# Performance work log

Measured on AMD Instinct MI355X. Metric: run time of the kernel, lower is better.

The kernel has to match this reference:

```python
import jax, jax.numpy as jnp
import numpy as np

N, E = 50000, 800000
IN, HID, H, OUT = 128, 32, 4, 32
NEG_SLOPE = 0.2


def _gatv2_layer(x, edge_index, Wl, bl, Wr, br, att, bias, heads, ch, concat):
    """One GATv2Conv layer (PyG semantics: add self-loops, lin_l on source,
    lin_r on target, e = att . leaky_relu(gl_src + gr_dst), segment softmax
    over incoming edges of each target, scatter-add weighted source messages)."""
    n = x.shape[0]
    loop = jnp.arange(n)
    src = jnp.concatenate([edge_index[0], loop])
    dst = jnp.concatenate([edge_index[1], loop])

    gl = (x @ Wl + bl).reshape(n, heads, ch)   # source transform [N,H,C]
    gr = (x @ Wr + br).reshape(n, heads, ch)   # target transform [N,H,C]

    m = jax.nn.leaky_relu(gl[src] + gr[dst], NEG_SLOPE)   # [E+N,H,C]
    e = jnp.einsum('ehc,hc->eh', m, att)                   # [E+N,H]

    # numerically stable segment softmax over dst
    emax = jax.lax.stop_gradient(jax.ops.segment_max(e, dst, num_segments=n))
    ex = jnp.exp(e - emax[dst])
    denom = jax.ops.segment_sum(ex, dst, num_segments=n)
    alpha = ex / denom[dst]                                # [E+N,H]

    out = jax.ops.segment_sum(alpha[:, :, None] * gl[src], dst, num_segments=n)  # [N,H,C]
    out = out.reshape(n, heads * ch) if concat else out.mean(axis=1)
    return out + bias


def setup_inputs() -> dict:
    key = jax.random.key(0)
    ks = jax.random.split(key, 16)
    s = 0.05
    return {
        'x': jax.random.normal(ks[0], (N, IN), dtype=jnp.float32),
        'edge_index': jax.random.randint(ks[1], (2, E), 0, N, dtype=jnp.int32),
        # layer 1: IN -> HID, H heads, concat
        'Wl1': jax.random.normal(ks[2], (IN, H * HID), dtype=jnp.float32) * s,
        'bl1': jnp.zeros((H * HID,), dtype=jnp.float32),
        'Wr1': jax.random.normal(ks[3], (IN, H * HID), dtype=jnp.float32) * s,
        'br1': jnp.zeros((H * HID,), dtype=jnp.float32),
        'att1': jax.random.normal(ks[4], (H, HID), dtype=jnp.float32) * s,
        'bias1': jnp.zeros((H * HID,), dtype=jnp.float32),
        # layer 2: H*HID -> OUT, 1 head, no concat
        'Wl2': jax.random.normal(ks[5], (H * HID, OUT), dtype=jnp.float32) * s,
        'bl2': jnp.zeros((OUT,), dtype=jnp.float32),
        'Wr2': jax.random.normal(ks[6], (H * HID, OUT), dtype=jnp.float32) * s,
        'br2': jnp.zeros((OUT,), dtype=jnp.float32),
        'att2': jax.random.normal(ks[7], (1, OUT), dtype=jnp.float32) * s,
        'bias2': jnp.zeros((OUT,), dtype=jnp.float32),
    }


def reference(x, edge_index, Wl1, bl1, Wr1, br1, att1, bias1,
              Wl2, bl2, Wr2, br2, att2, bias2):
    h = jax.nn.elu(_gatv2_layer(x, edge_index, Wl1, bl1, Wr1, br1, att1, bias1, H, HID, True))
    # dropout inactive in eval mode
    return _gatv2_layer(h, edge_index, Wl2, bl2, Wr2, br2, att2, bias2, 1, OUT, False)
```

## Files before the change

### kernel.cpp

```cpp
#include <hip/hip_runtime.h>

#define NNODES 50000
#define NEDGES 800000
#define ETOT   (NNODES + NEDGES)
#define NEG 0.2f
#define BKTS 196
#define P1E 4096
#define NP1 ((ETOT + P1E - 1) / P1E)

typedef unsigned short ushort_t;
typedef unsigned int uint_t;
typedef __attribute__((ext_vector_type(8))) short short8;
typedef __attribute__((ext_vector_type(4))) float f32x4;

__device__ __forceinline__ ushort_t f2bf(float f) {
  uint_t u = __float_as_uint(f);
  u += 0x7FFFu + ((u >> 16) & 1u);
  return (ushort_t)(u >> 16);
}
__device__ __forceinline__ float bf2f(ushort_t h) {
  return __uint_as_float((uint_t)h << 16);
}

__global__ __launch_bounds__(256) void coarse_hist(const int* __restrict__ ei,
                                                   int* __restrict__ pcnt) {
  __shared__ int c[BKTS];
  for (int i = threadIdx.x; i < BKTS; i += 256) c[i] = 0;
  __syncthreads();
  int e0 = blockIdx.x * P1E;
#pragma unroll
  for (int t = 0; t < P1E / 256; ++t) {
    int i = e0 + t * 256 + (int)threadIdx.x;
    if (i < ETOT) {
      int dst = (i < NEDGES) ? ei[NEDGES + i] : (i - NEDGES);
      atomicAdd(&c[dst >> 8], 1);
    }
  }
  __syncthreads();
  for (int i = threadIdx.x; i < BKTS; i += 256)
    pcnt[i * NP1 + blockIdx.x] = c[i];
}

__global__ __launch_bounds__(64) void coarse_scan(const int* __restrict__ pcnt,
                                                  int* __restrict__ goffArr,
                                                  int* __restrict__ tot) {
  int b = blockIdx.x;
  int lane = threadIdx.x;
  int carry = 0;
  for (int k0 = 0; k0 < NP1; k0 += 64) {
    int k = k0 + lane;
    int v = (k < NP1) ? pcnt[b * NP1 + k] : 0;
    int s = v;
    for (int off = 1; off < 64; off <<= 1) {
      int u = __shfl_up(s, off);
      if (lane >= off) s += u;
    }
    if (k < NP1) goffArr[b * NP1 + k] = carry + s - v;
    carry += __shfl(s, 63);
  }
  if (lane == 0) tot[b] = carry;
}

__global__ __launch_bounds__(256) void bucket_scan(const int* __restrict__ tot,
                                                   int* __restrict__ bucketStart,
                                                   int* __restrict__ rowptr) {
  if (threadIdx.x == 0) {
    int r = 0;
    for (int i = 0; i < BKTS; ++i) { bucketStart[i] = r; r += tot[i]; }
    bucketStart[BKTS] = r;
    rowptr[NNODES] = ETOT;
  }
}

__global__ __launch_bounds__(256) void bin_phase1(const int* __restrict__ ei,
                                                  const int* __restrict__ bucketStart,
                                                  const int* __restrict__ goffArr,
                                                  uint_t* __restrict__ binned) {
  __shared__ int cnt[BKTS], pref[BKTS], fillL[BKTS];
  __shared__ uint_t stage[P1E];
  int e0 = blockIdx.x * P1E;
  for (int i = threadIdx.x; i < BKTS; i += 256) { cnt[i] = 0; fillL[i] = 0; }
  __syncthreads();
  uint_t mypk[P1E / 256];
  int mybkt[P1E / 256];
#pragma unroll
  for (int t = 0; t < P1E / 256; ++t) {
    int i = e0 + t * 256 + (int)threadIdx.x;
    if (i < ETOT) {
      int dst = (i < NEDGES) ? ei[NEDGES + i] : (i - NEDGES);
      int src = (i < NEDGES) ? ei[i] : dst;
      int b = dst >> 8;
      mypk[t] = (uint_t)src | ((uint_t)(dst & 255) << 16) | ((uint_t)b << 24);
      mybkt[t] = b;
      atomicAdd(&cnt[b], 1);
    } else mybkt[t] = -1;
  }
  __syncthreads();
  if (threadIdx.x == 0) {
    int r = 0;
    for (int b = 0; b < BKTS; ++b) { pref[b] = r; r += cnt[b]; }
  }
  __syncthreads();
#pragma unroll
  for (int t = 0; t < P1E / 256; ++t) {
    if (mybkt[t] >= 0) {
      int p = pref[mybkt[t]] + atomicAdd(&fillL[mybkt[t]], 1);
      stage[p] = mypk[t];
    }
  }
  __syncthreads();
  int total = (e0 + P1E <= ETOT) ? P1E : (ETOT - e0);
  for (int j = threadIdx.x; j < total; j += 256) {
    uint_t pk = stage[j];
    int b = pk >> 24;
    binned[bucketStart[b] + goffArr[b * NP1 + blockIdx.x] + (j - pref[b])] = pk;
  }
}

__global__ __launch_bounds__(256) void bin_phase2(const uint_t* __restrict__ binned,
                                                  const int* __restrict__ bucketStart,
                                                  int* __restrict__ rowptr,
                                                  int* __restrict__ csrc) {
  __shared__ int cnt[256], pref[256], fillL[256];
  __shared__ int outS[8192];
  int b = blockIdx.x;
  int base = bucketStart[b];
  int cntAll = bucketStart[b + 1] - base;
  cnt[threadIdx.x] = 0; fillL[threadIdx.x] = 0;
  __syncthreads();
  for (int j = threadIdx.x; j < cntAll; j += 256)
    atomicAdd(&cnt[(binned[base + j] >> 16) & 255], 1);
  __syncthreads();
  if (threadIdx.x == 0) {
    int r = 0;
    for (int i = 0; i < 256; ++i) { pref[i] = r; r += cnt[i]; }
  }
  __syncthreads();
  int node = b * 256 + (int)threadIdx.x;
  if (node < NNODES) rowptr[node] = base + pref[threadIdx.x];
  for (int j = threadIdx.x; j < cntAll; j += 256) {
    uint_t pk = binned[base + j];
    int d = (pk >> 16) & 255;
    int p = pref[d] + atomicAdd(&fillL[d], 1);
    outS[p] = (int)(pk & 0xFFFF);
  }
  __syncthreads();
  for (int j = threadIdx.x; j < cntAll; j += 256)
    csrc[base + j] = outS[j];
}

__global__ __launch_bounds__(256) void prep_w(const float* __restrict__ Wl1,
                                              const float* __restrict__ Wr1,
                                              ushort_t* __restrict__ WtHi,
                                              ushort_t* __restrict__ WtLo) {
  int k = blockIdx.x;
  int n = threadIdx.x;
  float w = (n < 128) ? Wl1[k * 128 + n] : Wr1[k * 128 + (n - 128)];
  ushort_t h = f2bf(w);
  WtHi[n * 128 + k] = h;
  WtLo[n * 128 + k] = f2bf(w - bf2f(h));
}

__global__ __launch_bounds__(256) void gemm1_mfma(
    const float* __restrict__ x,
    const ushort_t* __restrict__ WtHi, const ushort_t* __restrict__ WtLo,
    const float* __restrict__ bl1, const float* __restrict__ br1,
    ushort_t* __restrict__ gl1, ushort_t* __restrict__ gr1) {
  constexpr int LDA = 132;
  __shared__ __align__(16) char smem[32 * 260 * 4];
  ushort_t (*Ahi)[LDA] = (ushort_t(*)[LDA])smem;
  ushort_t (*Alo)[LDA] = (ushort_t(*)[LDA])(smem + 32 * LDA * 2);
  float (*Cs)[260] = (float(*)[260])smem;
  int m0 = blockIdx.x * 32;
  int tid = threadIdx.x;
#pragma unroll
  for (int i = 0; i < 4; ++i) {
    int it = i * 256 + tid;
    int row = it >> 5, c4 = it & 31;
    int gm = m0 + row;
    float4 v = (gm < NNODES) ? *(const float4*)&x[(size_t)gm * 128 + 4 * c4]
                             : make_float4(0.f, 0.f, 0.f, 0.f);
    ushort_t h0 = f2bf(v.x), h1 = f2bf(v.y), h2 = f2bf(v.z), h3 = f2bf(v.w);
    ushort_t l0 = f2bf(v.x - bf2f(h0)), l1 = f2bf(v.y - bf2f(h1));
    ushort_t l2 = f2bf(v.z - bf2f(h2)), l3 = f2bf(v.w - bf2f(h3));
    uint2 ph, pl;
    ph.x = (uint_t)h0 | ((uint_t)h1 << 16); ph.y = (uint_t)h2 | ((uint_t)h3 << 16);
    pl.x = (uint_t)l0 | ((uint_t)l1 << 16); pl.y = (uint_t)l2 | ((uint_t)l3 << 16);
    *(uint2*)&Ahi[row][4 * c4] = ph;
    *(uint2*)&Alo[row][4 * c4] = pl;
  }
  __syncthreads();
  int wave = tid >> 6, lane = tid & 63;
  int quad = lane >> 4, nl = lane & 15;
  int nb = wave * 64;
  f32x4 acc[2][4];
#pragma unroll
  for (int tm = 0; tm < 2; ++tm)
#pragma unroll
    for (int tn = 0; tn < 4; ++tn) acc[tm][tn] = (f32x4){0.f, 0.f, 0.f, 0.f};

#pragma unroll
  for (int kc = 0; kc < 4; ++kc) {
    int klane = kc * 32 + quad * 8;
    short8 ah[2], al[2], bh[4], bl[4];
#pragma unroll
    for (int tm = 0; tm < 2; ++tm) {
      ah[tm] = *(const short8*)&Ahi[16 * tm + nl][klane];
      al[tm] = *(const short8*)&Alo[16 * tm + nl][klane];
    }
#pragma unroll
    for (int tn = 0; tn < 4; ++tn) {
      size_t wo = (size_t)(nb + 16 * tn + nl) * 128 + klane;
      bh[tn] = *(const short8*)&WtHi[wo];
      bl[tn] = *(const short8*)&WtLo[wo];
    }
#pragma unroll
    for (int tm = 0; tm < 2; ++tm)
#pragma unroll
      for (int tn = 0; tn < 4; ++tn) {
        acc[tm][tn] = __builtin_amdgcn_mfma_f32_16x16x32_bf16(ah[tm], bh[tn], acc[tm][tn], 0, 0, 0);
        acc[tm][tn] = __builtin_amdgcn_mfma_f32_16x16x32_bf16(ah[tm], bl[tn], acc[tm][tn], 0, 0, 0);
        acc[tm][tn] = __builtin_amdgcn_mfma_f32_16x16x32_bf16(al[tm], bh[tn], acc[tm][tn], 0, 0, 0);
      }
  }
  float bb[4];
#pragma unroll
  for (int tn = 0; tn < 4; ++tn) {
    int n = nb + 16 * tn + nl;
    bb[tn] = (n < 128) ? bl1[n] : br1[n - 128];
  }
  __syncthreads();
#pragma unroll
  for (int tm = 0; tm < 2; ++tm)
#pragma unroll
    for (int tn = 0; tn < 4; ++tn)
#pragma unroll
      for (int r = 0; r < 4; ++r)
        Cs[16 * tm + 4 * quad + r][nb + 16 * tn + nl] = acc[tm][tn][r] + bb[tn];
  __syncthreads();
#pragma unroll
  for (int i = 0; i < 2; ++i) {
    int it = i * 256 + tid;
    int row = it >> 4, oc = (it & 15) * 8;
    int gm = m0 + row;
    if (gm < NNODES) {
      uint4 pk;
      pk.x = (uint_t)f2bf(Cs[row][oc + 0]) | ((uint_t)f2bf(Cs[row][oc + 1]) << 16);
      pk.y = (uint_t)f2bf(Cs[row][oc + 2]) | ((uint_t)f2bf(Cs[row][oc + 3]) << 16);
      pk.z = (uint_t)f2bf(Cs[row][oc + 4]) | ((uint_t)f2bf(Cs[row][oc + 5]) << 16);
      pk.w = (uint_t)f2bf(Cs[row][oc + 6]) | ((uint_t)f2bf(Cs[row][oc + 7]) << 16);
      *(uint4*)&gl1[(size_t)gm * 128 + oc] = pk;
    }
  }
#pragma unroll
  for (int i = 0; i < 2; ++i) {
    int it = i * 256 + tid;
    int row = it >> 4, oc = (it & 15) * 8;
    int gm = m0 + row;
    if (gm < NNODES) {
      uint4 pk;
      pk.x = (uint_t)f2bf(Cs[row][128 + oc + 0]) | ((uint_t)f2bf(Cs[row][128 + oc + 1]) << 16);
      pk.y = (uint_t)f2bf(Cs[row][128 + oc + 2]) | ((uint_t)f2bf(Cs[row][128 + oc + 3]) << 16);
      pk.z = (uint_t)f2bf(Cs[row][128 + oc + 4]) | ((uint_t)f2bf(Cs[row][128 + oc + 5]) << 16);
      pk.w = (uint_t)f2bf(Cs[row][128 + oc + 6]) | ((uint_t)f2bf(Cs[row][128 + oc + 7]) << 16);
      *(uint4*)&gr1[(size_t)gm * 128 + oc] = pk;
    }
  }
}

__global__ __launch_bounds__(128) void gemm2_tile(
    const ushort_t* __restrict__ A,
    const float* __restrict__ W1, const float* __restrict__ b1,
    const float* __restrict__ W2, const float* __restrict__ b2,
    ushort_t* __restrict__ G1, ushort_t* __restrict__ G2) {
  constexpr int K = 128, KC = 32, BM = 128, BN = 64, MCOLS = 32, NT = 128;
  constexpr int LDA = BM + 4;
  __shared__ float AsT[KC][LDA];
  __shared__ float Ws[KC][BN];
  int row0 = blockIdx.x * BM;
  int tid = threadIdx.x;
  int tx = tid % (BN / 8), ty = tid / (BN / 8);
  float acc[8][8];
#pragma unroll
  for (int i = 0; i < 8; ++i)
#pragma unroll
    for (int j = 0; j < 8; ++j) acc[i][j] = 0.f;

  for (int kc = 0; kc < K; kc += KC) {
#pragma unroll
    for (int item = tid; item < BM * (KC / 4); item += NT) {
      int r = item >> 3, f4 = item & 7;
      int grow = row0 + r;
      uint2 u = (grow < NNODES)
          ? *(const uint2*)&A[(size_t)grow * K + kc + 4 * f4]
          : make_uint2(0u, 0u);
      AsT[4 * f4 + 0][r] = __uint_as_float(u.x << 16);
      AsT[4 * f4 + 1][r] = __uint_as_float(u.x & 0xffff0000u);
      AsT[4 * f4 + 2][r] = __uint_as_float(u.y << 16);
      AsT[4 * f4 + 3][r] = __uint_as_float(u.y & 0xffff0000u);
    }
#pragma unroll
    for (int item = tid; item < KC * (BN / 4); item += NT) {
      int k = item / (BN / 4), c4 = item % (BN / 4);
      int ccat = 4 * c4;
      const float* src = (ccat < MCOLS)
          ? &W1[(size_t)(kc + k) * MCOLS + ccat]
          : &W2[(size_t)(kc + k) * MCOLS + ccat - MCOLS];
      *(float4*)&Ws[k][4 * c4] = *(const float4*)src;
    }
    __syncthreads();
#pragma unroll 8
    for (int k = 0; k < KC; ++k) {
      float4 a0 = *(const float4*)&AsT[k][4 * ty];
      float4 a1 = *(const float4*)&AsT[k][BM / 2 + 4 * ty];
      float4 w0 = *(const float4*)&Ws[k][4 * tx];
      float4 w1 = *(const float4*)&Ws[k][BN / 2 + 4 * tx];
      float av[8] = {a0.x, a0.y, a0.z, a0.w, a1.x, a1.y, a1.z, a1.w};
      float wv[8] = {w0.x, w0.y, w0.z, w0.w, w1.x, w1.y, w1.z, w1.w};
#pragma unroll
      for (int i = 0; i < 8; ++i)
#pragma unroll
        for (int j = 0; j < 8; ++j) acc[i][j] = fmaf(av[i], wv[j], acc[i][j]);
    }
    __syncthreads();
  }
#pragma unroll
  for (int i = 0; i < 8; ++i) {
    int row = row0 + (i < 4 ? 4 * ty + i : BM / 2 + 4 * ty + (i - 4));
    if (row >= NNODES) continue;
#pragma unroll
    for (int jj = 0; jj < 2; ++jj) {
      int ccat = (jj == 0 ? 4 * tx : BN / 2 + 4 * tx);
      float o0 = acc[i][4 * jj + 0], o1 = acc[i][4 * jj + 1];
      float o2 = acc[i][4 * jj + 2], o3 = acc[i][4 * jj + 3];
      if (ccat < MCOLS) {
        float4 bb = *(const float4*)&b1[ccat];
        uint2 pk;
        pk.x = (uint_t)f2bf(o0 + bb.x) | ((uint_t)f2bf(o1 + bb.y) << 16);
        pk.y = (uint_t)f2bf(o2 + bb.z) | ((uint_t)f2bf(o3 + bb.w) << 16);
        *(uint2*)&G1[(size_t)row * MCOLS + ccat] = pk;
      } else {
        int c = ccat - MCOLS;
        float4 bb = *(const float4*)&b2[c];
        uint2 pk;
        pk.x = (uint_t)f2bf(o0 + bb.x) | ((uint_t)f2bf(o1 + bb.y) << 16);
        pk.y = (uint_t)f2bf(o2 + bb.z) | ((uint_t)f2bf(o3 + bb.w) << 16);
        *(uint2*)&G2[(size_t)row * MCOLS + c] = pk;
      }
    }
  }
}

__global__ __launch_bounds__(256) void gat1_edge(const int* __restrict__ rowptr,
                          const int* __restrict__ csrc,
                          const ushort_t* __restrict__ glb,
                          const ushort_t* __restrict__ grb,
                          const float* __restrict__ att, const float* __restrict__ bias,
                          ushort_t* __restrict__ hout) {
  int node = blockIdx.x * 4 + (threadIdx.x >> 6);
  if (node >= NNODES) return;
  int lane = threadIdx.x & 63;
  int eslot = lane >> 4;
  int q = lane & 15;
  int c8 = q * 8;
  float4 av0 = *(const float4*)(att + c8);
  float4 av1 = *(const float4*)(att + c8 + 4);
  uint4 ug = *(const uint4*)(grb + (size_t)node * 128 + c8);
  float4 gr0, gr1v;
  gr0.x = __uint_as_float(ug.x << 16);  gr0.y = __uint_as_float(ug.x & 0xffff0000u);
  gr0.z = __uint_as_float(ug.y << 16);  gr0.w = __uint_as_float(ug.y & 0xffff0000u);
  gr1v.x = __uint_as_float(ug.z << 16); gr1v.y = __uint_as_float(ug.z & 0xffff0000u);
  gr1v.z = __uint_as_float(ug.w << 16); gr1v.w = __uint_as_float(ug.w & 0xffff0000u);
  int start = rowptr[node], end = rowptr[node + 1];
  float denom = 0.f;
  float4 A0 = make_float4(0.f, 0.f, 0.f, 0.f);
  float4 A1 = make_float4(0.f, 0.f, 0.f, 0.f);
  for (int b = start; b < end; b += 64) {
    int nb = end - b; if (nb > 64) nb = 64;
    int sidx = (lane < nb) ? csrc[b + lane] : 0;
    for (int j = 0; j < nb; j += 4) {
      bool pv = (j + eslot) < nb;
      int s = __shfl(sidx, j + eslot);
      uint4 up = *(const uint4*)(glb + (size_t)s * 128 + c8);
      float4 g0, g1;
      g0.x = __uint_as_float(up.x << 16);
      g0.y = __uint_as_float(up.x & 0xffff0000u);
      g0.z = __uint_as_float(up.y << 16);
      g0.w = __uint_as_float(up.y & 0xffff0000u);
      g1.x = __uint_as_float(up.z << 16);
      g1.y = __uint_as_float(up.z & 0xffff0000u);
      g1.z = __uint_as_float(up.w << 16);
      g1.w = __uint_as_float(up.w & 0xffff0000u);
      float t, v;
      t = g0.x + gr0.x; t = fmaxf(t, NEG * t); v = av0.x * t;
      t = g0.y + gr0.y; t = fmaxf(t, NEG * t); v = fmaf(av0.y, t, v);
      t = g0.z + gr0.z; t = fmaxf(t, NEG * t); v = fmaf(av0.z, t, v);
      t = g0.w + gr0.w; t = fmaxf(t, NEG * t); v = fmaf(av0.w, t, v);
      t = g1.x + gr1v.x; t = fmaxf(t, NEG * t); v = fmaf(av1.x, t, v);
      t = g1.y + gr1v.y; t = fmaxf(t, NEG * t); v = fmaf(av1.y, t, v);
      t = g1.z + gr1v.z; t = fmaxf(t, NEG * t); v = fmaf(av1.z, t, v);
      t = g1.w + gr1v.w; t = fmaxf(t, NEG * t); v = fmaf(av1.w, t, v);
      v += __shfl_xor(v, 1); v += __shfl_xor(v, 2);
      float ex = pv ? __expf(v) : 0.f;
      denom += ex;
      A0.x = fmaf(ex, g0.x, A0.x); A0.y = fmaf(ex, g0.y, A0.y);
      A0.z = fmaf(ex, g0.z, A0.z); A0.w = fmaf(ex, g0.w, A0.w);
      A1.x = fmaf(ex, g1.x, A1.x); A1.y = fmaf(ex, g1.y, A1.y);
      A1.z = fmaf(ex, g1.z, A1.z); A1.w = fmaf(ex, g1.w, A1.w);
    }
  }
  denom += __shfl_xor(denom, 16); denom += __shfl_xor(denom, 32);
  A0.x += __shfl_xor(A0.x, 16); A0.x += __shfl_xor(A0.x, 32);
  A0.y += __shfl_xor(A0.y, 16); A0.y += __shfl_xor(A0.y, 32);
  A0.z += __shfl_xor(A0.z, 16); A0.z += __shfl_xor(A0.z, 32);
  A0.w += __shfl_xor(A0.w, 16); A0.w += __shfl_xor(A0.w, 32);
  A1.x += __shfl_xor(A1.x, 16); A1.x += __shfl_xor(A1.x, 32);
  A1.y += __shfl_xor(A1.y, 16); A1.y += __shfl_xor(A1.y, 32);
  A1.z += __shfl_xor(A1.z, 16); A1.z += __shfl_xor(A1.z, 32);
  A1.w += __shfl_xor(A1.w, 16); A1.w += __shfl_xor(A1.w, 32);
  float inv = 1.f / denom;
  if (eslot == 0) {
    float4 bv = *(const float4*)(bias + c8);
    float o0 = A0.x * inv + bv.x, o1 = A0.y * inv + bv.y;
    float o2 = A0.z * inv + bv.z, o3 = A0.w * inv + bv.w;
    o0 = o0 > 0.f ? o0 : __expf(o0) - 1.f;
    o1 = o1 > 0.f ? o1 : __expf(o1) - 1.f;
    o2 = o2 > 0.f ? o2 : __expf(o2) - 1.f;
    o3 = o3 > 0.f ? o3 : __expf(o3) - 1.f;
    uint2 pk;
    pk.x = (uint_t)f2bf(o0) | ((uint_t)f2bf(o1) << 16);
    pk.y = (uint_t)f2bf(o2) | ((uint_t)f2bf(o3) << 16);
    *(uint2*)&hout[(size_t)node * 128 + c8] = pk;
  } else if (eslot == 1) {
    float4 bv = *(const float4*)(bias + c8 + 4);
    float o0 = A1.x * inv + bv.x, o1 = A1.y * inv + bv.y;
    float o2 = A1.z * inv + bv.z, o3 = A1.w * inv + bv.w;
    o0 = o0 > 0.f ? o0 : __expf(o0) - 1.f;
    o1 = o1 > 0.f ? o1 : __expf(o1) - 1.f;
    o2 = o2 > 0.f ? o2 : __expf(o2) - 1.f;
    o3 = o3 > 0.f ? o3 : __expf(o3) - 1.f;
    uint2 pk;
    pk.x = (uint_t)f2bf(o0) | ((uint_t)f2bf(o1) << 16);
    pk.y = (uint_t)f2bf(o2) | ((uint_t)f2bf(o3) << 16);
    *(uint2*)&hout[(size_t)node * 128 + c8 + 4] = pk;
  }
}

__global__ __launch_bounds__(256) void gat2_edge(const int* __restrict__ rowptr,
                          const int* __restrict__ csrc,
                          const ushort_t* __restrict__ gl, const ushort_t* __restrict__ gr,
                          const float* __restrict__ att, const float* __restrict__ bias,
                          float* __restrict__ out) {
  int node = blockIdx.x * 4 + (threadIdx.x >> 6);
  if (node >= NNODES) return;
  int lane = threadIdx.x & 63;
  int eslot = lane >> 3;
  int q = lane & 7;
  int c4 = q * 4;
  float4 avc = *(const float4*)(att + c4);
  uint2 ugr = *(const uint2*)(gr + (size_t)node * 32 + c4);
  float4 grd;
  grd.x = __uint_as_float(ugr.x << 16); grd.y = __uint_as_float(ugr.x & 0xffff0000u);
  grd.z = __uint_as_float(ugr.y << 16); grd.w = __uint_as_float(ugr.y & 0xffff0000u);
  int start = rowptr[node], end = rowptr[node + 1];
  float denom = 0.f;
  float4 A = make_float4(0.f, 0.f, 0.f, 0.f);
  for (int b = start; b < end; b += 64) {
    int nb = end - b; if (nb > 64) nb = 64;
    int sidx = (lane < nb) ? csrc[b + lane] : 0;
    for (int j = 0; j < nb; j += 8) {
      bool pv = (j + eslot) < nb;
      int s = __shfl(sidx, j + eslot);
      uint2 ug = *(const uint2*)(gl + (size_t)s * 32 + c4);
      float4 g;
      g.x = __uint_as_float(ug.x << 16); g.y = __uint_as_float(ug.x & 0xffff0000u);
      g.z = __uint_as_float(ug.y << 16); g.w = __uint_as_float(ug.y & 0xffff0000u);
      float t, v;
      t = g.x + grd.x; t = fmaxf(t, NEG * t); v = avc.x * t;
      t = g.y + grd.y; t = fmaxf(t, NEG * t); v = fmaf(avc.y, t, v);
      t = g.z + grd.z; t = fmaxf(t, NEG * t); v = fmaf(avc.z, t, v);
      t = g.w + grd.w; t = fmaxf(t, NEG * t); v = fmaf(avc.w, t, v);
      v += __shfl_xor(v, 1); v += __shfl_xor(v, 2); v += __shfl_xor(v, 4);
      float ex = pv ? __expf(v) : 0.f;
      denom += ex;
      A.x = fmaf(ex, g.x, A.x); A.y = fmaf(ex, g.y, A.y);
      A.z = fmaf(ex, g.z, A.z); A.w = fmaf(ex, g.w, A.w);
    }
  }
  denom += __shfl_xor(denom, 8); denom += __shfl_xor(denom, 16); denom += __shfl_xor(denom, 32);
  A.x += __shfl_xor(A.x, 8); A.x += __shfl_xor(A.x, 16); A.x += __shfl_xor(A.x, 32);
  A.y += __shfl_xor(A.y, 8); A.y += __shfl_xor(A.y, 16); A.y += __shfl_xor(A.y, 32);
  A.z += __shfl_xor(A.z, 8); A.z += __shfl_xor(A.z, 16); A.z += __shfl_xor(A.z, 32);
  A.w += __shfl_xor(A.w, 8); A.w += __shfl_xor(A.w, 16); A.w += __shfl_xor(A.w, 32);
  if (eslot == 0) {
    float4 bv = *(const float4*)(bias + c4);
    float inv = 1.f / denom;
    float4 o;
    o.x = A.x * inv + bv.x; o.y = A.y * inv + bv.y;
    o.z = A.z * inv + bv.z; o.w = A.w * inv + bv.w;
    *(float4*)(out + (size_t)node * 32 + c4) = o;
  }
}

extern "C" void kernel_launch(void* const* d_in, const int* in_sizes, int n_in,
                              void* d_out, int out_size, void* d_ws, size_t ws_size,
                              hipStream_t stream) {
  const float* x     = (const float*)d_in[0];
  const int*   ei    = (const int*)  d_in[1];
  const float* Wl1   = (const float*)d_in[2];
  const float* bl1   = (const float*)d_in[3];
  const float* Wr1   = (const float*)d_in[4];
  const float* br1   = (const float*)d_in[5];
  const float* att1  = (const float*)d_in[6];
  const float* bias1 = (const float*)d_in[7];
  const float* Wl2   = (const float*)d_in[8];
  const float* bl2   = (const float*)d_in[9];
  const float* Wr2   = (const float*)d_in[10];
  const float* br2   = (const float*)d_in[11];
  const float* att2  = (const float*)d_in[12];
  const float* bias2 = (const float*)d_in[13];
  float* out = (float*)d_out;

  char* w = (char*)d_ws;
  auto carve = [&](size_t bytes) {
    char* p = w;
    w += (bytes + 255) & ~(size_t)255;
    return p;
  };
  ushort_t* gl1 = (ushort_t*)carve((size_t)NNODES * 128 * 2);
  ushort_t* gr1 = (ushort_t*)carve((size_t)NNODES * 128 * 2);
  ushort_t* h   = (ushort_t*)carve((size_t)NNODES * 128 * 2);
  ushort_t* gl2 = (ushort_t*)carve((size_t)NNODES * 32 * 2);
  ushort_t* gr2 = (ushort_t*)carve((size_t)NNODES * 32 * 2);
  ushort_t* WtHi = (ushort_t*)carve((size_t)256 * 128 * 2);
  ushort_t* WtLo = (ushort_t*)carve((size_t)256 * 128 * 2);
  int* pcnt    = (int*)carve((size_t)NP1 * BKTS * 4);
  int* goffArr = (int*)carve((size_t)NP1 * BKTS * 4);
  int* tot     = (int*)carve((size_t)BKTS * 4);
  int* bucketStart = (int*)carve((size_t)(BKTS + 1) * 4);
  int* rowptr = (int*)carve((size_t)(NNODES + 1) * 4);
  uint_t* binned = (uint_t*)carve((size_t)ETOT * 4);
  int* csrc = (int*)carve((size_t)ETOT * 4);

  prep_w<<<128, 256, 0, stream>>>(Wl1, Wr1, WtHi, WtLo);
  coarse_hist<<<NP1, 256, 0, stream>>>(ei, pcnt);
  coarse_scan<<<BKTS, 64, 0, stream>>>(pcnt, goffArr, tot);
  bucket_scan<<<1, 256, 0, stream>>>(tot, bucketStart, rowptr);
  bin_phase1<<<NP1, 256, 0, stream>>>(ei, bucketStart, goffArr, binned);
  bin_phase2<<<BKTS, 256, 0, stream>>>(binned, bucketStart, rowptr, csrc);

  gemm1_mfma<<<(NNODES + 31) / 32, 256, 0, stream>>>(x, WtHi, WtLo, bl1, br1, gl1, gr1);
  gat1_edge<<<(NNODES + 3) / 4, 256, 0, stream>>>(rowptr, csrc, gl1, gr1, att1, bias1, h);
  gemm2_tile<<<(NNODES + 127) / 128, 128, 0, stream>>>(h, Wl2, bl2, Wr2, br2, gl2, gr2);
  gat2_edge<<<(NNODES + 3) / 4, 256, 0, stream>>>(rowptr, csrc, gl2, gr2, att2, bias2, out);
}
```

Measured before the change: 264.3 us.

## Decompose leaky_relu attention into linear per-node terms plus abs term

Rewrites leaky_relu(t) as 0.6*t + 0.4*|t|, so the linear part of the attention logit splits into per-node source and target scalars. These scalars are computed in the GEMM epilogues and stored as el/er arrays. The edge kernels then evaluate only the abs term per edge and add the precomputed scalars. This removes the max/multiply per channel but adds an extra scalar gather per edge. Also parallelises bucket_scan with a wave scan, shrinks edge-kernel blocks to 128 threads, and uses rcp for the denominator.

```diff
diff --git a/kernel.cpp b/kernel.cpp
--- a/kernel.cpp
+++ b/kernel.cpp
@@ -61,13 +61,24 @@
   if (lane == 0) tot[b] = carry;
 }
 
-__global__ __launch_bounds__(256) void bucket_scan(const int* __restrict__ tot,
-                                                   int* __restrict__ bucketStart,
-                                                   int* __restrict__ rowptr) {
-  if (threadIdx.x == 0) {
-    int r = 0;
-    for (int i = 0; i < BKTS; ++i) { bucketStart[i] = r; r += tot[i]; }
-    bucketStart[BKTS] = r;
+__global__ __launch_bounds__(64) void bucket_scan(const int* __restrict__ tot,
+                                                  int* __restrict__ bucketStart,
+                                                  int* __restrict__ rowptr) {
+  int lane = threadIdx.x;
+  int carry = 0;
+  for (int k0 = 0; k0 < BKTS; k0 += 64) {
+    int k = k0 + lane;
+    int v = (k < BKTS) ? tot[k] : 0;
+    int s = v;
+    for (int off = 1; off < 64; off <<= 1) {
+      int u = __shfl_up(s, off);
+      if (lane >= off) s += u;
+    }
+    if (k < BKTS) bucketStart[k] = carry + s - v;
+    carry += __shfl(s, 63);
+  }
+  if (lane == 0) {
+    bucketStart[BKTS] = carry;
     rowptr[NNODES] = ETOT;
   }
 }
@@ -165,7 +176,9 @@
     const float* __restrict__ x,
     const ushort_t* __restrict__ WtHi, const ushort_t* __restrict__ WtLo,
     const float* __restrict__ bl1, const float* __restrict__ br1,
-    ushort_t* __restrict__ gl1, ushort_t* __restrict__ gr1) {
+    const float* __restrict__ att,
+    ushort_t* __restrict__ gl1, ushort_t* __restrict__ gr1,
+    float* __restrict__ elt, float* __restrict__ ern) {
   constexpr int LDA = 132;
   __shared__ __align__(16) char smem[32 * 260 * 4];
   ushort_t (*Ahi)[LDA] = (ushort_t(*)[LDA])smem;
@@ -266,13 +279,36 @@
       *(uint4*)&gr1[(size_t)gm * 128 + oc] = pk;
     }
   }
+  {
+    int row = tid >> 3, part = tid & 7;
+    int gm = m0 + row;
+    if (gm < NNODES) {
+      int hh = part & 3;
+      int cbase = ((part & 4) ? 128 : 0) + hh * 32;
+      float accd = 0.f;
+#pragma unroll
+      for (int c = 0; c < 32; c += 4) {
+        float4 cv = *(const float4*)&Cs[row][cbase + c];
+        float4 av = *(const float4*)&att[hh * 32 + c];
+        accd = fmaf(cv.x, av.x, accd);
+        accd = fmaf(cv.y, av.y, accd);
+        accd = fmaf(cv.z, av.z, accd);
+        accd = fmaf(cv.w, av.w, accd);
+      }
+      accd *= 0.6f;
+      if (part < 4) elt[gm * 4 + hh] = accd;
+      else          ern[gm * 4 + hh] = accd;
+    }
+  }
 }
 
 __global__ __launch_bounds__(128) void gemm2_tile(
     const ushort_t* __restrict__ A,
     const float* __restrict__ W1, const float* __restrict__ b1,
     const float* __restrict__ W2, const float* __restrict__ b2,
-    ushort_t* __restrict__ G1, ushort_t* __restrict__ G2) {
+    const float* __restrict__ att,
+    ushort_t* __restrict__ G1, ushort_t* __restrict__ G2,
+    float* __restrict__ el2, float* __restrict__ er2) {
   constexpr int K = 128, KC = 32, BM = 128, BN = 64, MCOLS = 32, NT = 128;
   constexpr int LDA = BM + 4;
   __shared__ float AsT[KC][LDA];
@@ -324,10 +360,13 @@
     }
     __syncthreads();
   }
+  float4 a6 = *(const float4*)&att[4 * tx];
+  a6.x *= 0.6f; a6.y *= 0.6f; a6.z *= 0.6f; a6.w *= 0.6f;
 #pragma unroll
   for (int i = 0; i < 8; ++i) {
     int row = row0 + (i < 4 ? 4 * ty + i : BM / 2 + 4 * ty + (i - 4));
     if (row >= NNODES) continue;
+    float pel = 0.f, per2 = 0.f;
 #pragma unroll
     for (int jj = 0; jj < 2; ++jj) {
       int ccat = (jj == 0 ? 4 * tx : BN / 2 + 4 * tx);
@@ -335,53 +374,74 @@
       float o2 = acc[i][4 * jj + 2], o3 = acc[i][4 * jj + 3];
       if (ccat < MCOLS) {
         float4 bb = *(const float4*)&b1[ccat];
+        o0 += bb.x; o1 += bb.y; o2 += bb.z; o3 += bb.w;
+        pel = fmaf(o0, a6.x, pel); pel = fmaf(o1, a6.y, pel);
+        pel = fmaf(o2, a6.z, pel); pel = fmaf(o3, a6.w, pel);
         uint2 pk;
-        pk.x = (uint_t)f2bf(o0 + bb.x) | ((uint_t)f2bf(o1 + bb.y) << 16);
-        pk.y = (uint_t)f2bf(o2 + bb.z) | ((uint_t)f2bf(o3 + bb.w) << 16);
+        pk.x = (uint_t)f2bf(o0) | ((uint_t)f2bf(o1) << 16);
+        pk.y = (uint_t)f2bf(o2) | ((uint_t)f2bf(o3) << 16);
         *(uint2*)&G1[(size_t)row * MCOLS + ccat] = pk;
       } else {
         int c = ccat - MCOLS;
         float4 bb = *(const float4*)&b2[c];
+        o0 += bb.x; o1 += bb.y; o2 += bb.z; o3 += bb.w;
+        per2 = fmaf(o0, a6.x, per2); per2 = fmaf(o1, a6.y, per2);
+        per2 = fmaf(o2, a6.z, per2); per2 = fmaf(o3, a6.w, per2);
         uint2 pk;
-        pk.x = (uint_t)f2bf(o0 + bb.x) | ((uint_t)f2bf(o1 + bb.y) << 16);
-        pk.y = (uint_t)f2bf(o2 + bb.z) | ((uint_t)f2bf(o3 + bb.w) << 16);
+        pk.x = (uint_t)f2bf(o0) | ((uint_t)f2bf(o1) << 16);
+        pk.y = (uint_t)f2bf(o2) | ((uint_t)f2bf(o3) << 16);
         *(uint2*)&G2[(size_t)row * MCOLS + c] = pk;
       }
     }
-  }
-}
-
-__global__ __launch_bounds__(256) void gat1_edge(const int* __restrict__ rowptr,
+    pel  += __shfl_xor(pel, 1);  pel  += __shfl_xor(pel, 2);  pel  += __shfl_xor(pel, 4);
+    per2 += __shfl_xor(per2, 1); per2 += __shfl_xor(per2, 2); per2 += __shfl_xor(per2, 4);
+    if (tx == 0) { el2[row] = pel; er2[row] = per2; }
+  }
+}
+
+__global__ __launch_bounds__(128) void gat1_edge(const int* __restrict__ rowptr,
                           const int* __restrict__ csrc,
                           const ushort_t* __restrict__ glb,
                           const ushort_t* __restrict__ grb,
+                          const float* __restrict__ elt,
+                          const float* __restrict__ ern,
                           const float* __restrict__ att, const float* __restrict__ bias,
                           ushort_t* __restrict__ hout) {
-  int node = blockIdx.x * 4 + (threadIdx.x >> 6);
+  int node = blockIdx.x * 2 + (threadIdx.x >> 6);
   if (node >= NNODES) return;
   int lane = threadIdx.x & 63;
   int eslot = lane >> 4;
   int q = lane & 15;
   int c8 = q * 8;
-  float4 av0 = *(const float4*)(att + c8);
-  float4 av1 = *(const float4*)(att + c8 + 4);
+  int head = q >> 2;
+  float4 a0 = *(const float4*)(att + c8);
+  float4 a1 = *(const float4*)(att + c8 + 4);
+  a0.x *= 0.4f; a0.y *= 0.4f; a0.z *= 0.4f; a0.w *= 0.4f;
+  a1.x *= 0.4f; a1.y *= 0.4f; a1.z *= 0.4f; a1.w *= 0.4f;
   uint4 ug = *(const uint4*)(grb + (size_t)node * 128 + c8);
   float4 gr0, gr1v;
   gr0.x = __uint_as_float(ug.x << 16);  gr0.y = __uint_as_float(ug.x & 0xffff0000u);
   gr0.z = __uint_as_float(ug.y << 16);  gr0.w = __uint_as_float(ug.y & 0xffff0000u);
   gr1v.x = __uint_as_float(ug.z << 16); gr1v.y = __uint_as_float(ug.z & 0xffff0000u);
   gr1v.z = __uint_as_float(ug.w << 16); gr1v.w = __uint_as_float(ug.w & 0xffff0000u);
+  float eb = ern[node * 4 + head];
   int start = rowptr[node], end = rowptr[node + 1];
   float denom = 0.f;
   float4 A0 = make_float4(0.f, 0.f, 0.f, 0.f);
   float4 A1 = make_float4(0.f, 0.f, 0.f, 0.f);
+  const char* glc = (const char*)glb;
+  const char* elc = (const char*)elt;
+  uint_t coff = (uint_t)(c8 * 2);
+  uint_t hoff = (uint_t)(head * 4);
   for (int b = start; b < end; b += 64) {
     int nb = end - b; if (nb > 64) nb = 64;
     int sidx = (lane < nb) ? csrc[b + lane] : 0;
     for (int j = 0; j < nb; j += 4) {
-      bool pv = (j + eslot) < nb;
-      int s = __shfl(sidx, j + eslot);
-      uint4 up = *(const uint4*)(glb + (size_t)s * 128 + c8);
+      int jj = j + eslot;
+      bool pv = jj < nb;
+      int s = __shfl(sidx, jj);
+      float el_s = *(const float*)(elc + (((uint_t)s << 4) + hoff));
+      uint4 up = *(const uint4*)(glc + (((uint_t)s << 8) + coff));
       float4 g0, g1;
       g0.x = __uint_as_float(up.x << 16);
       g0.y = __uint_as_float(up.x & 0xffff0000u);
@@ -392,15 +452,16 @@
       g1.z = __uint_as_float(up.w << 16);
       g1.w = __uint_as_float(up.w & 0xffff0000u);
       float t, v;
-      t = g0.x + gr0.x; t = fmaxf(t, NEG * t); v = av0.x * t;
-      t = g0.y + gr0.y; t = fmaxf(t, NEG * t); v = fmaf(av0.y, t, v);
-      t = g0.z + gr0.z; t = fmaxf(t, NEG * t); v = fmaf(av0.z, t, v);
-      t = g0.w + gr0.w; t = fmaxf(t, NEG * t); v = fmaf(av0.w, t, v);
-      t = g1.x + gr1v.x; t = fmaxf(t, NEG * t); v = fmaf(av1.x, t, v);
-      t = g1.y + gr1v.y; t = fmaxf(t, NEG * t); v = fmaf(av1.y, t, v);
-      t = g1.z + gr1v.z; t = fmaxf(t, NEG * t); v = fmaf(av1.z, t, v);
-      t = g1.w + gr1v.w; t = fmaxf(t, NEG * t); v = fmaf(av1.w, t, v);
+      t = g0.x + gr0.x;  v = a0.x * fabsf(t);
+      t = g0.y + gr0.y;  v = fmaf(a0.y, fabsf(t), v);
+      t = g0.z + gr0.z;  v = fmaf(a0.z, fabsf(t), v);
+      t = g0.w + gr0.w;  v = fmaf(a0.w, fabsf(t), v);
+      t = g1.x + gr1v.x; v = fmaf(a1.x, fabsf(t), v);
+      t = g1.y + gr1v.y; v = fmaf(a1.y, fabsf(t), v);
+      t = g1.z + gr1v.z; v = fmaf(a1.z, fabsf(t), v);
+      t = g1.w + gr1v.w; v = fmaf(a1.w, fabsf(t), v);
       v += __shfl_xor(v, 1); v += __shfl_xor(v, 2);
+      v += el_s + eb;
       float ex = pv ? __expf(v) : 0.f;
       denom += ex;
       A0.x = fmaf(ex, g0.x, A0.x); A0.y = fmaf(ex, g0.y, A0.y);
@@ -418,7 +479,7 @@
   A1.y += __shfl_xor(A1.y, 16); A1.y += __shfl_xor(A1.y, 32);
   A1.z += __shfl_xor(A1.z, 16); A1.z += __shfl_xor(A1.z, 32);
   A1.w += __shfl_xor(A1.w, 16); A1.w += __shfl_xor(A1.w, 32);
-  float inv = 1.f / denom;
+  float inv = __builtin_amdgcn_rcpf(denom);
   if (eslot == 0) {
     float4 bv = *(const float4*)(bias + c8);
     float o0 = A0.x * inv + bv.x, o1 = A0.y * inv + bv.y;
@@ -446,41 +507,49 @@
   }
 }
 
-__global__ __launch_bounds__(256) void gat2_edge(const int* __restrict__ rowptr,
+__global__ __launch_bounds__(128) void gat2_edge(const int* __restrict__ rowptr,
                           const int* __restrict__ csrc,
                           const ushort_t* __restrict__ gl, const ushort_t* __restrict__ gr,
+                          const float* __restrict__ el2, const float* __restrict__ er2,
                           const float* __restrict__ att, const float* __restrict__ bias,
                           float* __restrict__ out) {
-  int node = blockIdx.x * 4 + (threadIdx.x >> 6);
+  int node = blockIdx.x * 2 + (threadIdx.x >> 6);
   if (node >= NNODES) return;
   int lane = threadIdx.x & 63;
   int eslot = lane >> 3;
   int q = lane & 7;
   int c4 = q * 4;
   float4 avc = *(const float4*)(att + c4);
+  avc.x *= 0.4f; avc.y *= 0.4f; avc.z *= 0.4f; avc.w *= 0.4f;
   uint2 ugr = *(const uint2*)(gr + (size_t)node * 32 + c4);
   float4 grd;
   grd.x = __uint_as_float(ugr.x << 16); grd.y = __uint_as_float(ugr.x & 0xffff0000u);
   grd.z = __uint_as_float(ugr.y << 16); grd.w = __uint_as_float(ugr.y & 0xffff0000u);
+  float eb = er2[node];
   int start = rowptr[node], end = rowptr[node + 1];
   float denom = 0.f;
   float4 A = make_float4(0.f, 0.f, 0.f, 0.f);
+  const char* glc = (const char*)gl;
+  uint_t coff = (uint_t)(c4 * 2);
   for (int b = start; b < end; b += 64) {
     int nb = end - b; if (nb > 64) nb = 64;
     int sidx = (lane < nb) ? csrc[b + lane] : 0;
     for (int j = 0; j < nb; j += 8) {
-      bool pv = (j + eslot) < nb;
-      int s = __shfl(sidx, j + eslot);
-      uint2 ug = *(const uint2*)(gl + (size_t)s * 32 + c4);
+      int jj = j + eslot;
+      bool pv = jj < nb;
+      int s = __shfl(sidx, jj);
+      float el_s = el2[s];
+      uint2 ugl = *(const uint2*)(glc + (((uint_t)s << 6) + coff));
       float4 g;
-      g.x = __uint_as_float(ug.x << 16); g.y = __uint_as_float(ug.x & 0xffff0000u);
-      g.z = __uint_as_float(ug.y << 16); g.w = __uint_as_float(ug.y & 0xffff0000u);
+      g.x = __uint_as_float(ugl.x << 16); g.y = __uint_as_float(ugl.x & 0xffff0000u);
+      g.z = __uint_as_float(ugl.y << 16); g.w = __uint_as_float(ugl.y & 0xffff0000u);
       float t, v;
-      t = g.x + grd.x; t = fmaxf(t, NEG * t); v = avc.x * t;
-      t = g.y + grd.y; t = fmaxf(t, NEG * t); v = fmaf(avc.y, t, v);
-      t = g.z + grd.z; t = fmaxf(t, NEG * t); v = fmaf(avc.z, t, v);
-      t = g.w + grd.w; t = fmaxf(t, NEG * t); v = fmaf(avc.w, t, v);
+      t = g.x + grd.x; v = avc.x * fabsf(t);
+      t = g.y + grd.y; v = fmaf(avc.y, fabsf(t), v);
+      t = g.z + grd.z; v = fmaf(avc.z, fabsf(t), v);
+      t = g.w + grd.w; v = fmaf(avc.w, fabsf(t), v);
       v += __shfl_xor(v, 1); v += __shfl_xor(v, 2); v += __shfl_xor(v, 4);
+      v += el_s + eb;
       float ex = pv ? __expf(v) : 0.f;
       denom += ex;
       A.x = fmaf(ex, g.x, A.x); A.y = fmaf(ex, g.y, A.y);
@@ -493,8 +562,8 @@
   A.z += __shfl_xor(A.z, 8); A.z += __shfl_xor(A.z, 16); A.z += __shfl_xor(A.z, 32);
   A.w += __shfl_xor(A.w, 8); A.w += __shfl_xor(A.w, 16); A.w += __shfl_xor(A.w, 32);
   if (eslot == 0) {
+    float inv = __builtin_amdgcn_rcpf(denom);
     float4 bv = *(const float4*)(bias + c4);
-    float inv = 1.f / denom;
     float4 o;
     o.x = A.x * inv + bv.x; o.y = A.y * inv + bv.y;
     o.z = A.z * inv + bv.z; o.w = A.w * inv + bv.w;
@@ -534,6 +603,10 @@
   ushort_t* gr2 = (ushort_t*)carve((size_t)NNODES * 32 * 2);
   ushort_t* WtHi = (ushort_t*)carve((size_t)256 * 128 * 2);
   ushort_t* WtLo = (ushort_t*)carve((size_t)256 * 128 * 2);
+  float* elt = (float*)carve((size_t)NNODES * 4 * 4);
+  float* ern = (float*)carve((size_t)NNODES * 4 * 4);
+  float* el2 = (float*)carve((size_t)NNODES * 4);
+  float* er2 = (float*)carve((size_t)NNODES * 4);
   int* pcnt    = (int*)carve((size_t)NP1 * BKTS * 4);
   int* goffArr = (int*)carve((size_t)NP1 * BKTS * 4);
   int* tot     = (int*)carve((size_t)BKTS * 4);
@@ -545,12 +618,16 @@
   prep_w<<<128, 256, 0, stream>>>(Wl1, Wr1, WtHi, WtLo);
   coarse_hist<<<NP1, 256, 0, stream>>>(ei, pcnt);
   coarse_scan<<<BKTS, 64, 0, stream>>>(pcnt, goffArr, tot);
-  bucket_scan<<<1, 256, 0, stream>>>(tot, bucketStart, rowptr);
+  bucket_scan<<<1, 64, 0, stream>>>(tot, bucketStart, rowptr);
   bin_phase1<<<NP1, 256, 0, stream>>>(ei, bucketStart, goffArr, binned);
   bin_phase2<<<BKTS, 256, 0, stream>>>(binned, bucketStart, rowptr, csrc);
 
-  gemm1_mfma<<<(NNODES + 31) / 32, 256, 0, stream>>>(x, WtHi, WtLo, bl1, br1, gl1, gr1);
-  gat1_edge<<<(NNODES + 3) / 4, 256, 0, stream>>>(rowptr, csrc, gl1, gr1, att1, bias1, h);
-  gemm2_tile<<<(NNODES + 127) / 128, 128, 0, stream>>>(h, Wl2, bl2, Wr2, br2, gl2, gr2);
-  gat2_edge<<<(NNODES + 3) / 4, 256, 0, stream>>>(rowptr, csrc, gl2, gr2, att2, bias2, out);
-}
+  gemm1_mfma<<<(NNODES + 31) / 32, 256, 0, stream>>>(x, WtHi, WtLo, bl1, br1, att1,
+                                                     gl1, gr1, elt, ern);
+  gat1_edge<<<(NNODES + 1) / 2, 128, 0, stream>>>(rowptr, csrc, gl1, gr1, elt, ern,
+                                                  att1, bias1, h);
+  gemm2_tile<<<(NNODES + 127) / 128, 128, 0, stream>>>(h, Wl2, bl2, Wr2, br2, att2,
+                                                       gl2, gr2, el2, er2);
+  gat2_edge<<<(NNODES + 1) / 2, 128, 0, stream>>>(rowptr, csrc, gl2, gr2, el2, er2,
+                                                  att2, bias2, out);
+}
```

After: 271.8 us. 2.8% more time.
